# Kernel optimization log

Measured on AMD Instinct MI355X. Metric: run time of the kernel, lower is better.

Reference implementation:

```python
import jax, jax.numpy as jnp
import numpy as np

N_NODES = 100000
N_EDGES = 3200000
N_GRAPHS = 64
IN_DIM = 128
HID = 64
NUM_FAMILIES = 64
CPF = 3  # centroids per family
GOODWARE_C = 5
BN_EPS = 1e-5


def setup_inputs() -> dict:
    key = jax.random.key(0)
    ks = jax.random.split(key, 16)
    x = jax.random.normal(ks[0], (N_NODES, IN_DIM), dtype=jnp.float32)
    edge_index = jax.random.randint(ks[1], (2, N_EDGES), 0, N_NODES, dtype=jnp.int32)
    batch = jnp.sort(jax.random.randint(ks[2], (N_NODES,), 0, N_GRAPHS, dtype=jnp.int32))
    def lin(k, fin, fout):
        s = 1.0 / np.sqrt(fin)
        return jax.random.uniform(k, (fin, fout), jnp.float32, -s, s)
    W1 = lin(ks[3], IN_DIM, HID); b1 = jnp.zeros((HID,), jnp.float32)
    W2 = lin(ks[4], HID, HID);    b2 = jnp.zeros((HID,), jnp.float32)
    W3 = lin(ks[5], HID, HID);    b3 = jnp.zeros((HID,), jnp.float32)
    g1 = jnp.ones((HID,), jnp.float32); be1 = jnp.zeros((HID,), jnp.float32)
    g2 = jnp.ones((HID,), jnp.float32); be2 = jnp.zeros((HID,), jnp.float32)
    g3 = jnp.ones((HID,), jnp.float32); be3 = jnp.zeros((HID,), jnp.float32)
    cm = jax.random.normal(ks[6], (NUM_FAMILIES * CPF, HID), jnp.float32) / np.sqrt(HID)
    cg = jax.random.normal(ks[7], (GOODWARE_C, HID), jnp.float32) / np.sqrt(HID)
    temp = jnp.ones((1,), jnp.float32)
    return dict(x=x, edge_index=edge_index, batch=batch,
                W1=W1, b1=b1, g1=g1, be1=be1,
                W2=W2, b2=b2, g2=g2, be2=be2,
                W3=W3, b3=b3, g3=g3, be3=be3,
                cg=cg, cm=cm, temp=temp)


def _gcn_conv(h_in, W, b, row, col, dinv_sqrt):
    # GCNConv: lin -> symmetric-normalized scatter-add (with self loops) -> bias
    h = h_in @ W  # [N, HID]
    enorm = (dinv_sqrt[row] * dinv_sqrt[col])[:, None]  # [E, 1]
    agg = jax.ops.segment_sum(h[row] * enorm, col, num_segments=N_NODES)
    agg = agg + h * (dinv_sqrt * dinv_sqrt)[:, None]  # self-loop term (norm = 1/deg)
    return agg + b


def _bn(x, gamma, beta):
    # training-mode BatchNorm1d over node dim (biased variance)
    m = jnp.mean(x, axis=0)
    v = jnp.mean((x - m) ** 2, axis=0)
    return (x - m) * jax.lax.rsqrt(v + BN_EPS) * gamma + beta


def reference(x, edge_index, batch,
              W1, b1, g1, be1, W2, b2, g2, be2, W3, b3, g3, be3,
              cg, cm, temp):
    row, col = edge_index[0], edge_index[1]
    # degree including self loop
    deg = jax.ops.segment_sum(jnp.ones((N_EDGES,), jnp.float32), col,
                              num_segments=N_NODES) + 1.0
    dinv_sqrt = jax.lax.rsqrt(deg)

    h = jax.nn.relu(_bn(_gcn_conv(x, W1, b1, row, col, dinv_sqrt), g1, be1))
    h = jax.nn.relu(_bn(_gcn_conv(h, W2, b2, row, col, dinv_sqrt), g2, be2))
    h = _bn(_gcn_conv(h, W3, b3, row, col, dinv_sqrt), g3, be3)

    # global mean pool over graphs
    sums = jax.ops.segment_sum(h, batch, num_segments=N_GRAPHS)
    cnts = jax.ops.segment_sum(jnp.ones((N_NODES,), jnp.float32), batch,
                               num_segments=N_GRAPHS)
    emb = sums / jnp.maximum(cnts, 1.0)[:, None]  # [B, HID]

    # centroid classifier (phase='family')
    gd = jnp.sum((emb[:, None, :] - cg[None, :, :]) ** 2, axis=2)  # [B, 5]
    md = jnp.sum((emb[:, None, :] - cm[None, :, :]) ** 2, axis=2)  # [B, F*CPF]
    md = md.reshape(N_GRAPHS, NUM_FAMILIES, CPF)
    min_g = jnp.min(gd, axis=1)          # [B]
    min_m = jnp.min(md, axis=2)          # [B, F]
    logits = jnp.concatenate([(-min_g / temp)[:, None], -min_m / temp], axis=1)
    return logits
```

## Files before the change

### kernel.cpp

```cpp
#include <hip/hip_runtime.h>
#include <math.h>

#define N_NODES 100000
#define N_EDGES 3200000
#define N_GRAPHS 64
#define IN_DIM 128
#define HID 64
#define BN_EPS 1e-5f

#define PSHIFT 9
#define PBS 512
#define NPB ((N_NODES + PBS - 1) / PBS)
#define PART_BLOCKS 256
#define CHUNK_E (N_EDGES / PART_BLOCKS)

#define QBOUND 25000
#define AGG_BLOCKS 2048

typedef unsigned short ushort_t;
typedef __attribute__((ext_vector_type(8))) short bf16x8;
typedef __attribute__((ext_vector_type(4))) float f32x4;

__device__ __forceinline__ float bflo(unsigned u) { return __uint_as_float(u << 16); }
__device__ __forceinline__ float bfhi(unsigned u) { return __uint_as_float(u & 0xFFFF0000u); }
__device__ __forceinline__ float bfu(ushort_t u) { return __uint_as_float((unsigned)u << 16); }
__device__ __forceinline__ unsigned f2bf(float f) {
  unsigned u = __float_as_uint(f);
  return (u + 0x7FFFu + ((u >> 16) & 1u)) >> 16;
}


__global__ __launch_bounds__(256) void ghist_k(const int* __restrict__ ei,
                                               int* __restrict__ gh) {
  __shared__ int h[NPB];
  for (int i = threadIdx.x; i < NPB; i += 256) h[i] = 0;
  __syncthreads();
  const int4* d4 = (const int4*)(ei + N_EDGES);
  int n4 = N_EDGES / 4;
  int stride = gridDim.x * 256;
  for (int i = blockIdx.x * 256 + threadIdx.x; i < n4; i += stride) {
    int4 d = d4[i];
    atomicAdd(&h[d.x >> PSHIFT], 1);
    atomicAdd(&h[d.y >> PSHIFT], 1);
    atomicAdd(&h[d.z >> PSHIFT], 1);
    atomicAdd(&h[d.w >> PSHIFT], 1);
  }
  __syncthreads();
  for (int i = threadIdx.x; i < NPB; i += 256) {
    int v = h[i];
    if (v) atomicAdd(&gh[i], v);
  }
}

__global__ __launch_bounds__(256) void gscan_k(const int* __restrict__ gh,
                                               int* __restrict__ boff,
                                               int* __restrict__ gcur) {
  __shared__ int sa[256], sb[256];
  int t = threadIdx.x;
  int v = (t < NPB) ? gh[t] : 0;
  sa[t] = v;
  __syncthreads();
  int* src = sa; int* dst = sb;
  for (int o = 1; o < 256; o <<= 1) {
    dst[t] = src[t] + ((t >= o) ? src[t - o] : 0);
    __syncthreads();
    int* tmp = src; src = dst; dst = tmp;
  }
  if (t < NPB) {
    int excl = src[t] - v;
    boff[t] = excl;
    gcur[t] = excl;
    if (t == NPB - 1) boff[NPB] = src[t];
  }
}

__global__ __launch_bounds__(512) void part_k(const int* __restrict__ ei,
                                              int* __restrict__ gcur,
                                              unsigned* __restrict__ tmp) {
  __shared__ int lh[NPB];
  __shared__ int lcur[NPB];
  int t = threadIdx.x;
  for (int i = t; i < NPB; i += 512) lh[i] = 0;
  __syncthreads();
  int q0 = blockIdx.x * (CHUNK_E / 4);
  int q1 = q0 + CHUNK_E / 4;
  const int4* d4 = (const int4*)(ei + N_EDGES);
  const int4* s4 = (const int4*)ei;
  for (int i = q0 + t; i < q1; i += 512) {
    int4 d = d4[i];
    atomicAdd(&lh[d.x >> PSHIFT], 1);
    atomicAdd(&lh[d.y >> PSHIFT], 1);
    atomicAdd(&lh[d.z >> PSHIFT], 1);
    atomicAdd(&lh[d.w >> PSHIFT], 1);
  }
  __syncthreads();
  for (int i = t; i < NPB; i += 512) {
    int v = lh[i];
    lcur[i] = v ? atomicAdd(&gcur[i], v) : 0;
  }
  __syncthreads();
  for (int i = q0 + t; i < q1; i += 512) {
    int4 d = d4[i];
    int4 s = s4[i];
    int b0 = d.x >> PSHIFT, b1 = d.y >> PSHIFT, b2 = d.z >> PSHIFT, b3 = d.w >> PSHIFT;
    int p0 = atomicAdd(&lcur[b0], 1);
    int p1 = atomicAdd(&lcur[b1], 1);
    int p2 = atomicAdd(&lcur[b2], 1);
    int p3 = atomicAdd(&lcur[b3], 1);
    tmp[p0] = ((unsigned)(d.x & (PBS - 1)) << 17) | (unsigned)s.x;
    tmp[p1] = ((unsigned)(d.y & (PBS - 1)) << 17) | (unsigned)s.y;
    tmp[p2] = ((unsigned)(d.z & (PBS - 1)) << 17) | (unsigned)s.z;
    tmp[p3] = ((unsigned)(d.w & (PBS - 1)) << 17) | (unsigned)s.w;
  }
}

__global__ __launch_bounds__(512) void bwork_k(
    const unsigned* __restrict__ tmp, const int* __restrict__ boff,
    int* __restrict__ rp4, float* __restrict__ dinv, int* __restrict__ csr) {
  int b = blockIdx.x;
  int base = boff[b], end = boff[b + 1];
  int t = threadIdx.x;
  __shared__ int cnt[PBS * 4];
  __shared__ int cur[PBS * 4];
  __shared__ int sa[PBS], sb[PBS];
  for (int i = t; i < PBS * 4; i += 512) cnt[i] = 0;
  __syncthreads();
  int a0 = (base + 3) & ~3;
  int a1 = end & ~3;
  if (a1 < a0) { a0 = end; a1 = end; }
  const uint4* t4 = (const uint4*)tmp;
#define HIST1(U) { unsigned u_ = (U); int nl_ = u_ >> 17; int s_ = u_ & 0x1FFFF; \
    int qq_ = (s_ >= QBOUND) + (s_ >= 2*QBOUND) + (s_ >= 3*QBOUND); \
    atomicAdd(&cnt[nl_ * 4 + qq_], 1); }
  if (base + t < a0) HIST1(tmp[base + t]);
  for (int i = a0 / 4 + t; i < a1 / 4; i += 512) {
    uint4 u = t4[i];
    HIST1(u.x) HIST1(u.y) HIST1(u.z) HIST1(u.w)
  }
  if (a1 + t < end) HIST1(tmp[a1 + t]);
#undef HIST1
  __syncthreads();
  int c0 = cnt[t * 4], c1 = cnt[t * 4 + 1], c2 = cnt[t * 4 + 2], c3 = cnt[t * 4 + 3];
  int tsum = c0 + c1 + c2 + c3;
  sa[t] = tsum;
  __syncthreads();
  int* src_ = sa; int* dst_ = sb;
  for (int o = 1; o < PBS; o <<= 1) {
    dst_[t] = src_[t] + ((t >= o) ? src_[t - o] : 0);
    __syncthreads();
    int* z = src_; src_ = dst_; dst_ = z;
  }
  int nb = src_[t] - tsum;
  int o0 = nb, o1 = nb + c0, o2 = nb + c0 + c1, o3 = nb + c0 + c1 + c2;
  cur[t * 4] = o0; cur[t * 4 + 1] = o1; cur[t * 4 + 2] = o2; cur[t * 4 + 3] = o3;
  int n = b * PBS + t;
  if (n < N_NODES) {
    rp4[4 * n] = base + o0;
    rp4[4 * n + 1] = base + o1;
    rp4[4 * n + 2] = base + o2;
    rp4[4 * n + 3] = base + o3;
    dinv[n] = rsqrtf((float)(tsum + 1));
    if (n == N_NODES - 1) rp4[4 * N_NODES] = base + nb + tsum;
  }
  __syncthreads();
#define PLACE1(U) { unsigned u_ = (U); int nl_ = u_ >> 17; int s_ = u_ & 0x1FFFF; \
    int qq_ = (s_ >= QBOUND) + (s_ >= 2*QBOUND) + (s_ >= 3*QBOUND); \
    int p_ = atomicAdd(&cur[nl_ * 4 + qq_], 1); \
    csr[base + p_] = s_ << 7; }
  if (base + t < a0) PLACE1(tmp[base + t]);
  for (int i = a0 / 4 + t; i < a1 / 4; i += 512) {
    uint4 u = t4[i];
    PLACE1(u.x) PLACE1(u.y) PLACE1(u.z) PLACE1(u.w)
  }
  if (a1 + t < end) PLACE1(tmp[a1 + t]);
#undef PLACE1
}


template <int K, bool XBF16, bool APPLY, bool RELU>
__global__ __launch_bounds__(256) void gemm_k(
    const void* __restrict__ Xv, const float* __restrict__ W,
    const float* __restrict__ sums, const float* __restrict__ gamma,
    const float* __restrict__ beta, const float* __restrict__ dinv,
    ushort_t* __restrict__ out, int nrows) {
  __shared__ ushort_t wt[64 * K];
  __shared__ float scs[128], shs[128];
  __shared__ float redo[64 * 65];
  const int tid = threadIdx.x;
  const int wv = tid >> 6;
  const int lane = tid & 63;
  const int lm = lane & 15;
  const int lq = lane >> 4;

  for (int idx = tid; idx < K * 64; idx += 256) {
    int k = idx >> 6, c = idx & 63;
    wt[c * K + k] = (ushort_t)f2bf(W[idx]);
  }
  if (APPLY) {
    for (int k = tid; k < K; k += 256) {
      float m = sums[k] / (float)N_NODES;
      float v = sums[64 + k] / (float)N_NODES - m * m;
      float s = gamma[k] * rsqrtf(v + BN_EPS);
      scs[k] = s;
      shs[k] = beta[k] - m * s;
    }
  }
  __syncthreads();

  const int rowbase = blockIdx.x * 64;
  const int grow = rowbase + wv * 16 + lm;
  const bool valid = grow < nrows;
  f32x4 acc0 = {0.f, 0.f, 0.f, 0.f};
  f32x4 acc1 = acc0, acc2 = acc0, acc3 = acc0;

#pragma unroll
  for (int k0 = 0; k0 < K; k0 += 32) {
    int kbase = k0 + lq * 8;
    bf16x8 a = {0, 0, 0, 0, 0, 0, 0, 0};
    if (valid) {
      if (XBF16) {
        uint4 u = *(const uint4*)((const char*)Xv + ((size_t)grow * 64 + kbase) * 2);
        if (APPLY) {
          float4 sc0 = *(const float4*)&scs[kbase];
          float4 sc1 = *(const float4*)&scs[kbase + 4];
          float4 sh0 = *(const float4*)&shs[kbase];
          float4 sh1 = *(const float4*)&shs[kbase + 4];
          float f0 = bflo(u.x) * sc0.x + sh0.x, f1 = bfhi(u.x) * sc0.y + sh0.y;
          float f2 = bflo(u.y) * sc0.z + sh0.z, f3 = bfhi(u.y) * sc0.w + sh0.w;
          float f4 = bflo(u.z) * sc1.x + sh1.x, f5 = bfhi(u.z) * sc1.y + sh1.y;
          float f6 = bflo(u.w) * sc1.z + sh1.z, f7 = bfhi(u.w) * sc1.w + sh1.w;
          if (RELU) {
            f0 = fmaxf(f0, 0.f); f1 = fmaxf(f1, 0.f);
            f2 = fmaxf(f2, 0.f); f3 = fmaxf(f3, 0.f);
            f4 = fmaxf(f4, 0.f); f5 = fmaxf(f5, 0.f);
            f6 = fmaxf(f6, 0.f); f7 = fmaxf(f7, 0.f);
          }
          a[0] = (short)f2bf(f0); a[1] = (short)f2bf(f1);
          a[2] = (short)f2bf(f2); a[3] = (short)f2bf(f3);
          a[4] = (short)f2bf(f4); a[5] = (short)f2bf(f5);
          a[6] = (short)f2bf(f6); a[7] = (short)f2bf(f7);
        } else {
          a = *(const bf16x8*)&u;
        }
      } else {
        const float* xp = (const float*)Xv + (size_t)grow * K + kbase;
        float4 xa = *(const float4*)xp;
        float4 xb = *(const float4*)(xp + 4);
        a[0] = (short)f2bf(xa.x); a[1] = (short)f2bf(xa.y);
        a[2] = (short)f2bf(xa.z); a[3] = (short)f2bf(xa.w);
        a[4] = (short)f2bf(xb.x); a[5] = (short)f2bf(xb.y);
        a[6] = (short)f2bf(xb.z); a[7] = (short)f2bf(xb.w);
      }
    }
    bf16x8 b0 = *(const bf16x8*)(wt + (0 + lm) * K + kbase);
    bf16x8 b1 = *(const bf16x8*)(wt + (16 + lm) * K + kbase);
    bf16x8 b2 = *(const bf16x8*)(wt + (32 + lm) * K + kbase);
    bf16x8 b3 = *(const bf16x8*)(wt + (48 + lm) * K + kbase);
    acc0 = __builtin_amdgcn_mfma_f32_16x16x32_bf16(a, b0, acc0, 0, 0, 0);
    acc1 = __builtin_amdgcn_mfma_f32_16x16x32_bf16(a, b1, acc1, 0, 0, 0);
    acc2 = __builtin_amdgcn_mfma_f32_16x16x32_bf16(a, b2, acc2, 0, 0, 0);
    acc3 = __builtin_amdgcn_mfma_f32_16x16x32_bf16(a, b3, acc3, 0, 0, 0);
  }

#pragma unroll
  for (int r = 0; r < 4; ++r) {
    int rr = wv * 16 + lq * 4 + r;
    redo[rr * 65 + lm] = acc0[r];
    redo[rr * 65 + 16 + lm] = acc1[r];
    redo[rr * 65 + 32 + lm] = acc2[r];
    redo[rr * 65 + 48 + lm] = acc3[r];
  }
  __syncthreads();
  {
    int r = tid >> 2;
    int cq = (tid & 3) * 16;
    int gr = rowbase + r;
    if (gr < nrows) {
      float dn = dinv[gr];
      const float* sp = &redo[r * 65 + cq];
      unsigned p[8];
#pragma unroll
      for (int i = 0; i < 8; ++i)
        p[i] = f2bf(sp[2 * i] * dn) | (f2bf(sp[2 * i + 1] * dn) << 16);
      char* ob = (char*)out + ((size_t)gr * 64 + cq) * 2;
      *(uint4*)ob = make_uint4(p[0], p[1], p[2], p[3]);
      *(uint4*)(ob + 16) = make_uint4(p[4], p[5], p[6], p[7]);
    }
  }
}


__global__ __launch_bounds__(256) void agg_k(
    const ushort_t* __restrict__ hs, const float* __restrict__ dinv,
    const int* __restrict__ rp4, const int* __restrict__ csr,
    const float* __restrict__ bias, ushort_t* __restrict__ out,
    float* __restrict__ sums) {
  const int tid = threadIdx.x;
  const int w = tid >> 6;
  const int lane = tid & 63;
  const int g = lane >> 4;
  const int q = lane & 15;
  const char* hb = (const char*)hs;
  char* ob = (char*)out;

  float4 bval = *(const float4*)(bias + q * 4);
  float4 s = make_float4(0.f, 0.f, 0.f, 0.f);
  float4 s2 = make_float4(0.f, 0.f, 0.f, 0.f);

  for (int n = blockIdx.x * 16 + w * 4 + g; n < N_NODES; n += AGG_BLOCKS * 16) {
    int r0 = rp4[4 * n];
    int cnt = rp4[4 * n + 4] - r0;
    uint2 selfu = *(const uint2*)(hb + ((size_t)n << 7) + (q << 3));
    float4 aA = {0, 0, 0, 0}, aB = {0, 0, 0, 0};
    int j = 0;
    if (cnt >= 8) {
      int e0 = csr[r0 + 0], e1 = csr[r0 + 1], e2 = csr[r0 + 2], e3 = csr[r0 + 3];
      int e4 = csr[r0 + 4], e5 = csr[r0 + 5], e6 = csr[r0 + 6], e7 = csr[r0 + 7];
      for (; j + 16 <= cnt; j += 8) {
        uint2 v0 = *(const uint2*)(hb + (size_t)(unsigned)e0 + (q << 3));
        uint2 v1 = *(const uint2*)(hb + (size_t)(unsigned)e1 + (q << 3));
        uint2 v2 = *(const uint2*)(hb + (size_t)(unsigned)e2 + (q << 3));
        uint2 v3 = *(const uint2*)(hb + (size_t)(unsigned)e3 + (q << 3));
        uint2 v4 = *(const uint2*)(hb + (size_t)(unsigned)e4 + (q << 3));
        uint2 v5 = *(const uint2*)(hb + (size_t)(unsigned)e5 + (q << 3));
        uint2 v6 = *(const uint2*)(hb + (size_t)(unsigned)e6 + (q << 3));
        uint2 v7 = *(const uint2*)(hb + (size_t)(unsigned)e7 + (q << 3));
        e0 = csr[r0 + j + 8];  e1 = csr[r0 + j + 9];
        e2 = csr[r0 + j + 10]; e3 = csr[r0 + j + 11];
        e4 = csr[r0 + j + 12]; e5 = csr[r0 + j + 13];
        e6 = csr[r0 + j + 14]; e7 = csr[r0 + j + 15];
        aA.x += bflo(v0.x); aA.y += bfhi(v0.x); aA.z += bflo(v0.y); aA.w += bfhi(v0.y);
        aB.x += bflo(v1.x); aB.y += bfhi(v1.x); aB.z += bflo(v1.y); aB.w += bfhi(v1.y);
        aA.x += bflo(v2.x); aA.y += bfhi(v2.x); aA.z += bflo(v2.y); aA.w += bfhi(v2.y);
        aB.x += bflo(v3.x); aB.y += bfhi(v3.x); aB.z += bflo(v3.y); aB.w += bfhi(v3.y);
        aA.x += bflo(v4.x); aA.y += bfhi(v4.x); aA.z += bflo(v4.y); aA.w += bfhi(v4.y);
        aB.x += bflo(v5.x); aB.y += bfhi(v5.x); aB.z += bflo(v5.y); aB.w += bfhi(v5.y);
        aA.x += bflo(v6.x); aA.y += bfhi(v6.x); aA.z += bflo(v6.y); aA.w += bfhi(v6.y);
        aB.x += bflo(v7.x); aB.y += bfhi(v7.x); aB.z += bflo(v7.y); aB.w += bfhi(v7.y);
      }
      {
        uint2 v0 = *(const uint2*)(hb + (size_t)(unsigned)e0 + (q << 3));
        uint2 v1 = *(const uint2*)(hb + (size_t)(unsigned)e1 + (q << 3));
        uint2 v2 = *(const uint2*)(hb + (size_t)(unsigned)e2 + (q << 3));
        uint2 v3 = *(const uint2*)(hb + (size_t)(unsigned)e3 + (q << 3));
        uint2 v4 = *(const uint2*)(hb + (size_t)(unsigned)e4 + (q << 3));
        uint2 v5 = *(const uint2*)(hb + (size_t)(unsigned)e5 + (q << 3));
        uint2 v6 = *(const uint2*)(hb + (size_t)(unsigned)e6 + (q << 3));
        uint2 v7 = *(const uint2*)(hb + (size_t)(unsigned)e7 + (q << 3));
        aA.x += bflo(v0.x); aA.y += bfhi(v0.x); aA.z += bflo(v0.y); aA.w += bfhi(v0.y);
        aB.x += bflo(v1.x); aB.y += bfhi(v1.x); aB.z += bflo(v1.y); aB.w += bfhi(v1.y);
        aA.x += bflo(v2.x); aA.y += bfhi(v2.x); aA.z += bflo(v2.y); aA.w += bfhi(v2.y);
        aB.x += bflo(v3.x); aB.y += bfhi(v3.x); aB.z += bflo(v3.y); aB.w += bfhi(v3.y);
        aA.x += bflo(v4.x); aA.y += bfhi(v4.x); aA.z += bflo(v4.y); aA.w += bfhi(v4.y);
        aB.x += bflo(v5.x); aB.y += bfhi(v5.x); aB.z += bflo(v5.y); aB.w += bfhi(v5.y);
        aA.x += bflo(v6.x); aA.y += bfhi(v6.x); aA.z += bflo(v6.y); aA.w += bfhi(v6.y);
        aB.x += bflo(v7.x); aB.y += bfhi(v7.x); aB.z += bflo(v7.y); aB.w += bfhi(v7.y);
        j += 8;
      }
    }
    for (; j + 2 <= cnt; j += 2) {
      int e0 = csr[r0 + j + 0], e1 = csr[r0 + j + 1];
      uint2 v0 = *(const uint2*)(hb + (size_t)(unsigned)e0 + (q << 3));
      uint2 v1 = *(const uint2*)(hb + (size_t)(unsigned)e1 + (q << 3));
      aA.x += bflo(v0.x); aA.y += bfhi(v0.x); aA.z += bflo(v0.y); aA.w += bfhi(v0.y);
      aB.x += bflo(v1.x); aB.y += bfhi(v1.x); aB.z += bflo(v1.y); aB.w += bfhi(v1.y);
    }
    if (j < cnt) {
      int e0 = csr[r0 + j];
      uint2 v0 = *(const uint2*)(hb + (size_t)(unsigned)e0 + (q << 3));
      aA.x += bflo(v0.x); aA.y += bfhi(v0.x); aA.z += bflo(v0.y); aA.w += bfhi(v0.y);
    }
    float4 a;
    a.x = aA.x + aB.x + bflo(selfu.x);
    a.y = aA.y + aB.y + bfhi(selfu.x);
    a.z = aA.z + aB.z + bflo(selfu.y);
    a.w = aA.w + aB.w + bfhi(selfu.y);
    float dn = dinv[n];
    a.x = a.x * dn + bval.x; a.y = a.y * dn + bval.y;
    a.z = a.z * dn + bval.z; a.w = a.w * dn + bval.w;
    uint2 o;
    o.x = f2bf(a.x) | (f2bf(a.y) << 16);
    o.y = f2bf(a.z) | (f2bf(a.w) << 16);
    *(uint2*)(ob + ((size_t)n << 7) + (q << 3)) = o;
    s.x += a.x; s.y += a.y; s.z += a.z; s.w += a.w;
    s2.x += a.x * a.x; s2.y += a.y * a.y;
    s2.z += a.z * a.z; s2.w += a.w * a.w;
  }

  __shared__ float rs[16][64];
  __shared__ float rs2[16][64];
  *(float4*)(&rs[w * 4 + g][q * 4]) = s;
  *(float4*)(&rs2[w * 4 + g][q * 4]) = s2;
  __syncthreads();
  int c = tid & 63;
  int r0_ = tid >> 6;
  float a = rs[r0_][c] + rs[r0_ + 4][c] + rs[r0_ + 8][c] + rs[r0_ + 12][c];
  float a2 = rs2[r0_][c] + rs2[r0_ + 4][c] + rs2[r0_ + 8][c] + rs2[r0_ + 12][c];
  __syncthreads();
  rs[r0_][c] = a;
  rs2[r0_][c] = a2;
  __syncthreads();
  if (r0_ == 0) {
    atomicAdd(&sums[c], rs[0][c] + rs[1][c] + rs[2][c] + rs[3][c]);
    atomicAdd(&sums[64 + c], rs2[0][c] + rs2[1][c] + rs2[2][c] + rs2[3][c]);
  }
}


#define POOL_CHUNK 32
__global__ __launch_bounds__(256) void pool_k(
    const ushort_t* __restrict__ h, const float* __restrict__ sums,
    const float* __restrict__ gamma, const float* __restrict__ beta,
    const int* __restrict__ batch,
    float* __restrict__ psum, float* __restrict__ pcnt) {
  int w = threadIdx.x >> 6;
  int lane = threadIdx.x & 63;
  int start = (blockIdx.x * 4 + w) * POOL_CHUNK;
  if (start >= N_NODES) return;
  int end = min(start + POOL_CHUNK, N_NODES);
  float m = sums[lane] / (float)N_NODES;
  float v = sums[64 + lane] / (float)N_NODES - m * m;
  float sc = gamma[lane] * rsqrtf(v + BN_EPS);
  float sh = beta[lane] - m * sc;
  float acc = 0.f, cnt = 0.f;
  int cur = batch[start];
  for (int n = start; n < end; ++n) {
    int g = batch[n];
    if (g != cur) {
      atomicAdd(&psum[cur * 64 + lane], acc);
      if (lane == 0) atomicAdd(&pcnt[cur], cnt);
      acc = 0.f; cnt = 0.f; cur = g;
    }
    acc += bfu(h[(size_t)n * 64 + lane]) * sc + sh;
    cnt += 1.f;
  }
  atomicAdd(&psum[cur * 64 + lane], acc);
  if (lane == 0) atomicAdd(&pcnt[cur], cnt);
}


__global__ void classify_k(const float* __restrict__ psum, const float* __restrict__ pcnt,
                           const float* __restrict__ cg_, const float* __restrict__ cm,
                           const float* __restrict__ temp, float* __restrict__ out) {
  int g = blockIdx.x;
  int t = threadIdx.x;
  __shared__ float emb[64];
  __shared__ float dist[208];
  if (t < 64) emb[t] = psum[g * 64 + t] / fmaxf(pcnt[g], 1.0f);
  __syncthreads();
  if (t < 197) {
    const float* C = (t < 5) ? (cg_ + t * 64) : (cm + (t - 5) * 64);
    float d = 0.f;
#pragma unroll 8
    for (int k = 0; k < 64; ++k) {
      float df = emb[k] - C[k];
      d += df * df;
    }
    dist[t] = d;
  }
  __syncthreads();
  float tv = temp[0];
  if (t == 64) {
    float m = dist[0];
    for (int j = 1; j < 5; ++j) m = fminf(m, dist[j]);
    out[g * 65] = -m / tv;
  }
  if (t < 64) {
    float m = fminf(dist[5 + t * 3], fminf(dist[5 + t * 3 + 1], dist[5 + t * 3 + 2]));
    out[g * 65 + 1 + t] = -m / tv;
  }
}


extern "C" void kernel_launch(void* const* d_in, const int* in_sizes, int n_in,
                              void* d_out, int out_size, void* d_ws, size_t ws_size,
                              hipStream_t stream) {
  const float* x   = (const float*)d_in[0];
  const int* ei    = (const int*)d_in[1];
  const int* batch = (const int*)d_in[2];
  const float* W1 = (const float*)d_in[3];  const float* b1 = (const float*)d_in[4];
  const float* g1 = (const float*)d_in[5];  const float* be1 = (const float*)d_in[6];
  const float* W2 = (const float*)d_in[7];  const float* b2 = (const float*)d_in[8];
  const float* g2 = (const float*)d_in[9];  const float* be2 = (const float*)d_in[10];
  const float* W3 = (const float*)d_in[11]; const float* b3 = (const float*)d_in[12];
  const float* g3 = (const float*)d_in[13]; const float* be3 = (const float*)d_in[14];
  const float* cg_ = (const float*)d_in[15];
  const float* cm = (const float*)d_in[16];
  const float* temp = (const float*)d_in[17];
  float* out = (float*)d_out;

  char* ws = (char*)d_ws;
  size_t off = 0;
  auto alloc = [&](size_t bytes) -> void* {
    void* p = ws + off;
    off = (off + bytes + 255) & ~(size_t)255;
    return p;
  };
  int* gh        = (int*)alloc((size_t)NPB * 4);
  float* sumsAll = (float*)alloc(3 * 128 * 4);
  float* psum    = (float*)alloc(64 * 64 * 4);
  float* pcnt    = (float*)alloc(64 * 4);
  size_t zero_end = off;
  int* boff      = (int*)alloc((size_t)(NPB + 1) * 4);
  int* gcur      = (int*)alloc((size_t)NPB * 4);
  unsigned* tmp  = (unsigned*)alloc((size_t)N_EDGES * 4);
  int* csr       = (int*)alloc((size_t)N_EDGES * 4);
  int* rp4       = (int*)alloc((size_t)(4 * N_NODES + 1) * 4);
  float* dinv    = (float*)alloc((size_t)N_NODES * 4);
  ushort_t* hA   = (ushort_t*)alloc((size_t)N_NODES * 64 * 2);
  ushort_t* hB   = (ushort_t*)alloc((size_t)N_NODES * 64 * 2);

  hipMemsetAsync(ws, 0, zero_end, stream);

  const int NB_GEMM = (N_NODES + 63) / 64;
  const int NB_POOL = (N_NODES + POOL_CHUNK * 4 - 1) / (POOL_CHUNK * 4);

  ghist_k<<<512, 256, 0, stream>>>(ei, gh);
  gscan_k<<<1, 256, 0, stream>>>(gh, boff, gcur);
  part_k<<<PART_BLOCKS, 512, 0, stream>>>(ei, gcur, tmp);
  bwork_k<<<NPB, 512, 0, stream>>>(tmp, boff, rp4, dinv, csr);

  gemm_k<IN_DIM, false, false, false><<<NB_GEMM, 256, 0, stream>>>(x, W1, nullptr, nullptr, nullptr, dinv, hA, N_NODES);
  agg_k<<<AGG_BLOCKS, 256, 0, stream>>>(hA, dinv, rp4, csr, b1, hB, sumsAll);

  gemm_k<HID, true, true, true><<<NB_GEMM, 256, 0, stream>>>(hB, W2, sumsAll, g1, be1, dinv, hA, N_NODES);
  agg_k<<<AGG_BLOCKS, 256, 0, stream>>>(hA, dinv, rp4, csr, b2, hB, sumsAll + 128);

  gemm_k<HID, true, true, true><<<NB_GEMM, 256, 0, stream>>>(hB, W3, sumsAll + 128, g2, be2, dinv, hA, N_NODES);
  agg_k<<<AGG_BLOCKS, 256, 0, stream>>>(hA, dinv, rp4, csr, b3, hB, sumsAll + 256);

  pool_k<<<NB_POOL, 256, 0, stream>>>(hB, sumsAll + 256, g3, be3, batch, psum, pcnt);
  classify_k<<<N_GRAPHS, 256, 0, stream>>>(psum, pcnt, cg_, cm, temp, out);
}
```

Baseline: 545.0 us.

## Fuse pooling into last aggregation and restructure agg to per-thread node batches

The aggregation kernel now assigns four consecutive nodes to each 16-lane group, using one block per 64 nodes instead of a grid-stride loop. It reads the four partitioned row-pointer ranges with vector loads and walks each partition with an 8/4/2/1 unrolled gather. The final layer's aggregation accumulates per-graph sums into shared memory and flushes them with atomics, so the separate pool kernel and the write of the last hidden state go away. The BatchNorm affine is applied to the pooled mean in the classifier, since it is linear. The trade-offs are a 16KB shared buffer with its zeroing in the pooled variant, and loss of the two-accumulator software prefetching in the gather loop.

```diff
diff --git a/kernel.cpp b/kernel.cpp
--- a/kernel.cpp
+++ b/kernel.cpp
@@ -15,7 +15,7 @@
 #define CHUNK_E (N_EDGES / PART_BLOCKS)
 
 #define QBOUND 25000
-#define AGG_BLOCKS 2048
+#define NB_AGG ((N_NODES + 63) / 64)
 
 typedef unsigned short ushort_t;
 typedef __attribute__((ext_vector_type(8))) short bf16x8;
@@ -290,11 +290,13 @@
 }
 
 
+template <bool POOL>
 __global__ __launch_bounds__(256) void agg_k(
     const ushort_t* __restrict__ hs, const float* __restrict__ dinv,
     const int* __restrict__ rp4, const int* __restrict__ csr,
     const float* __restrict__ bias, ushort_t* __restrict__ out,
-    float* __restrict__ sums) {
+    float* __restrict__ sums, const int* __restrict__ batch,
+    float* __restrict__ psum, float* __restrict__ pcnt) {
   const int tid = threadIdx.x;
   const int w = tid >> 6;
   const int lane = tid & 63;
@@ -302,93 +304,147 @@
   const int q = lane & 15;
   const char* hb = (const char*)hs;
   char* ob = (char*)out;
-
+  const int qo = q << 3;
+
+  __shared__ float rs[16][64];
+  __shared__ float rs2[16][64];
+  __shared__ float pl[POOL ? 64 * 64 : 1];
+  __shared__ float pcl[POOL ? 64 : 1];
+  if (POOL) {
+    for (int i = tid; i < 64 * 64; i += 256) pl[i] = 0.f;
+    if (tid < 64) pcl[tid] = 0.f;
+    __syncthreads();
+  }
+
+  const int nb = blockIdx.x * 64 + (w * 4 + g) * 4;
+
+  int4 rp[4];
+  int en[4];
+#pragma unroll
+  for (int i = 0; i < 4; ++i) {
+    int n = nb + i;
+    if (n < N_NODES) {
+      rp[i] = *(const int4*)(rp4 + 4 * n);
+      en[i] = rp4[4 * n + 4];
+    } else {
+      rp[i] = make_int4(0, 0, 0, 0);
+      en[i] = 0;
+    }
+  }
   float4 bval = *(const float4*)(bias + q * 4);
+  float4 acc[4];
+#pragma unroll
+  for (int i = 0; i < 4; ++i) acc[i] = make_float4(0.f, 0.f, 0.f, 0.f);
+
+#define GV1(E, A) { uint2 v_ = *(const uint2*)(hb + (size_t)(unsigned)(E) + qo); \
+    A.x += bflo(v_.x); A.y += bfhi(v_.x); A.z += bflo(v_.y); A.w += bfhi(v_.y); }
+
+  for (int p = 0; p < 4; ++p) {
+#pragma unroll
+    for (int i = 0; i < 4; ++i) {
+      int lo = (p == 0) ? rp[i].x : (p == 1) ? rp[i].y : (p == 2) ? rp[i].z : rp[i].w;
+      int hi = (p == 3) ? en[i] : ((p == 0) ? rp[i].y : (p == 1) ? rp[i].z : rp[i].w);
+      float4 a4 = acc[i];
+      int jj = lo;
+      for (; jj + 8 <= hi; jj += 8) {
+        int e0 = csr[jj], e1 = csr[jj + 1], e2 = csr[jj + 2], e3 = csr[jj + 3];
+        int e4 = csr[jj + 4], e5 = csr[jj + 5], e6 = csr[jj + 6], e7 = csr[jj + 7];
+        uint2 v0 = *(const uint2*)(hb + (size_t)(unsigned)e0 + qo);
+        uint2 v1 = *(const uint2*)(hb + (size_t)(unsigned)e1 + qo);
+        uint2 v2 = *(const uint2*)(hb + (size_t)(unsigned)e2 + qo);
+        uint2 v3 = *(const uint2*)(hb + (size_t)(unsigned)e3 + qo);
+        uint2 v4 = *(const uint2*)(hb + (size_t)(unsigned)e4 + qo);
+        uint2 v5 = *(const uint2*)(hb + (size_t)(unsigned)e5 + qo);
+        uint2 v6 = *(const uint2*)(hb + (size_t)(unsigned)e6 + qo);
+        uint2 v7 = *(const uint2*)(hb + (size_t)(unsigned)e7 + qo);
+        a4.x += bflo(v0.x); a4.y += bfhi(v0.x); a4.z += bflo(v0.y); a4.w += bfhi(v0.y);
+        a4.x += bflo(v1.x); a4.y += bfhi(v1.x); a4.z += bflo(v1.y); a4.w += bfhi(v1.y);
+        a4.x += bflo(v2.x); a4.y += bfhi(v2.x); a4.z += bflo(v2.y); a4.w += bfhi(v2.y);
+        a4.x += bflo(v3.x); a4.y += bfhi(v3.x); a4.z += bflo(v3.y); a4.w += bfhi(v3.y);
+        a4.x += bflo(v4.x); a4.y += bfhi(v4.x); a4.z += bflo(v4.y); a4.w += bfhi(v4.y);
+        a4.x += bflo(v5.x); a4.y += bfhi(v5.x); a4.z += bflo(v5.y); a4.w += bfhi(v5.y);
+        a4.x += bflo(v6.x); a4.y += bfhi(v6.x); a4.z += bflo(v6.y); a4.w += bfhi(v6.y);
+        a4.x += bflo(v7.x); a4.y += bfhi(v7.x); a4.z += bflo(v7.y); a4.w += bfhi(v7.y);
+      }
+      if (jj + 4 <= hi) {
+        int e0 = csr[jj], e1 = csr[jj + 1], e2 = csr[jj + 2], e3 = csr[jj + 3];
+        uint2 v0 = *(const uint2*)(hb + (size_t)(unsigned)e0 + qo);
+        uint2 v1 = *(const uint2*)(hb + (size_t)(unsigned)e1 + qo);
+        uint2 v2 = *(const uint2*)(hb + (size_t)(unsigned)e2 + qo);
+        uint2 v3 = *(const uint2*)(hb + (size_t)(unsigned)e3 + qo);
+        a4.x += bflo(v0.x); a4.y += bfhi(v0.x); a4.z += bflo(v0.y); a4.w += bfhi(v0.y);
+        a4.x += bflo(v1.x); a4.y += bfhi(v1.x); a4.z += bflo(v1.y); a4.w += bfhi(v1.y);
+        a4.x += bflo(v2.x); a4.y += bfhi(v2.x); a4.z += bflo(v2.y); a4.w += bfhi(v2.y);
+        a4.x += bflo(v3.x); a4.y += bfhi(v3.x); a4.z += bflo(v3.y); a4.w += bfhi(v3.y);
+        jj += 4;
+      }
+      if (jj + 2 <= hi) {
+        int e0 = csr[jj], e1 = csr[jj + 1];
+        uint2 v0 = *(const uint2*)(hb + (size_t)(unsigned)e0 + qo);
+        uint2 v1 = *(const uint2*)(hb + (size_t)(unsigned)e1 + qo);
+        a4.x += bflo(v0.x); a4.y += bfhi(v0.x); a4.z += bflo(v0.y); a4.w += bfhi(v0.y);
+        a4.x += bflo(v1.x); a4.y += bfhi(v1.x); a4.z += bflo(v1.y); a4.w += bfhi(v1.y);
+        jj += 2;
+      }
+      if (jj < hi) {
+        GV1(csr[jj], a4)
+      }
+      acc[i] = a4;
+    }
+  }
+#undef GV1
+
   float4 s = make_float4(0.f, 0.f, 0.f, 0.f);
   float4 s2 = make_float4(0.f, 0.f, 0.f, 0.f);
-
-  for (int n = blockIdx.x * 16 + w * 4 + g; n < N_NODES; n += AGG_BLOCKS * 16) {
-    int r0 = rp4[4 * n];
-    int cnt = rp4[4 * n + 4] - r0;
-    uint2 selfu = *(const uint2*)(hb + ((size_t)n << 7) + (q << 3));
-    float4 aA = {0, 0, 0, 0}, aB = {0, 0, 0, 0};
-    int j = 0;
-    if (cnt >= 8) {
-      int e0 = csr[r0 + 0], e1 = csr[r0 + 1], e2 = csr[r0 + 2], e3 = csr[r0 + 3];
-      int e4 = csr[r0 + 4], e5 = csr[r0 + 5], e6 = csr[r0 + 6], e7 = csr[r0 + 7];
-      for (; j + 16 <= cnt; j += 8) {
-        uint2 v0 = *(const uint2*)(hb + (size_t)(unsigned)e0 + (q << 3));
-        uint2 v1 = *(const uint2*)(hb + (size_t)(unsigned)e1 + (q << 3));
-        uint2 v2 = *(const uint2*)(hb + (size_t)(unsigned)e2 + (q << 3));
-        uint2 v3 = *(const uint2*)(hb + (size_t)(unsigned)e3 + (q << 3));
-        uint2 v4 = *(const uint2*)(hb + (size_t)(unsigned)e4 + (q << 3));
-        uint2 v5 = *(const uint2*)(hb + (size_t)(unsigned)e5 + (q << 3));
-        uint2 v6 = *(const uint2*)(hb + (size_t)(unsigned)e6 + (q << 3));
-        uint2 v7 = *(const uint2*)(hb + (size_t)(unsigned)e7 + (q << 3));
-        e0 = csr[r0 + j + 8];  e1 = csr[r0 + j + 9];
-        e2 = csr[r0 + j + 10]; e3 = csr[r0 + j + 11];
-        e4 = csr[r0 + j + 12]; e5 = csr[r0 + j + 13];
-        e6 = csr[r0 + j + 14]; e7 = csr[r0 + j + 15];
-        aA.x += bflo(v0.x); aA.y += bfhi(v0.x); aA.z += bflo(v0.y); aA.w += bfhi(v0.y);
-        aB.x += bflo(v1.x); aB.y += bfhi(v1.x); aB.z += bflo(v1.y); aB.w += bfhi(v1.y);
-        aA.x += bflo(v2.x); aA.y += bfhi(v2.x); aA.z += bflo(v2.y); aA.w += bfhi(v2.y);
-        aB.x += bflo(v3.x); aB.y += bfhi(v3.x); aB.z += bflo(v3.y); aB.w += bfhi(v3.y);
-        aA.x += bflo(v4.x); aA.y += bfhi(v4.x); aA.z += bflo(v4.y); aA.w += bfhi(v4.y);
-        aB.x += bflo(v5.x); aB.y += bfhi(v5.x); aB.z += bflo(v5.y); aB.w += bfhi(v5.y);
-        aA.x += bflo(v6.x); aA.y += bfhi(v6.x); aA.z += bflo(v6.y); aA.w += bfhi(v6.y);
-        aB.x += bflo(v7.x); aB.y += bfhi(v7.x); aB.z += bflo(v7.y); aB.w += bfhi(v7.y);
+  int curg = -1, pcount = 0;
+  float4 pacc = make_float4(0.f, 0.f, 0.f, 0.f);
+#pragma unroll
+  for (int i = 0; i < 4; ++i) {
+    int n = nb + i;
+    if (n < N_NODES) {
+      uint2 su = *(const uint2*)(hb + ((size_t)n << 7) + qo);
+      float dn = dinv[n];
+      float4 a;
+      a.x = (acc[i].x + bflo(su.x)) * dn + bval.x;
+      a.y = (acc[i].y + bfhi(su.x)) * dn + bval.y;
+      a.z = (acc[i].z + bflo(su.y)) * dn + bval.z;
+      a.w = (acc[i].w + bfhi(su.y)) * dn + bval.w;
+      if (!POOL) {
+        uint2 o;
+        o.x = f2bf(a.x) | (f2bf(a.y) << 16);
+        o.y = f2bf(a.z) | (f2bf(a.w) << 16);
+        *(uint2*)(ob + ((size_t)n << 7) + qo) = o;
+      } else {
+        int gi = batch[n];
+        if (gi != curg) {
+          if (pcount) {
+            atomicAdd(&pl[curg * 64 + (q << 2)], pacc.x);
+            atomicAdd(&pl[curg * 64 + (q << 2) + 1], pacc.y);
+            atomicAdd(&pl[curg * 64 + (q << 2) + 2], pacc.z);
+            atomicAdd(&pl[curg * 64 + (q << 2) + 3], pacc.w);
+            if (q == 0) atomicAdd(&pcl[curg], (float)pcount);
+          }
+          curg = gi;
+          pacc = a;
+          pcount = 1;
+        } else {
+          pacc.x += a.x; pacc.y += a.y; pacc.z += a.z; pacc.w += a.w;
+          pcount++;
+        }
       }
-      {
-        uint2 v0 = *(const uint2*)(hb + (size_t)(unsigned)e0 + (q << 3));
-        uint2 v1 = *(const uint2*)(hb + (size_t)(unsigned)e1 + (q << 3));
-        uint2 v2 = *(const uint2*)(hb + (size_t)(unsigned)e2 + (q << 3));
-        uint2 v3 = *(const uint2*)(hb + (size_t)(unsigned)e3 + (q << 3));
-        uint2 v4 = *(const uint2*)(hb + (size_t)(unsigned)e4 + (q << 3));
-        uint2 v5 = *(const uint2*)(hb + (size_t)(unsigned)e5 + (q << 3));
-        uint2 v6 = *(const uint2*)(hb + (size_t)(unsigned)e6 + (q << 3));
-        uint2 v7 = *(const uint2*)(hb + (size_t)(unsigned)e7 + (q << 3));
-        aA.x += bflo(v0.x); aA.y += bfhi(v0.x); aA.z += bflo(v0.y); aA.w += bfhi(v0.y);
-        aB.x += bflo(v1.x); aB.y += bfhi(v1.x); aB.z += bflo(v1.y); aB.w += bfhi(v1.y);
-        aA.x += bflo(v2.x); aA.y += bfhi(v2.x); aA.z += bflo(v2.y); aA.w += bfhi(v2.y);
-        aB.x += bflo(v3.x); aB.y += bfhi(v3.x); aB.z += bflo(v3.y); aB.w += bfhi(v3.y);
-        aA.x += bflo(v4.x); aA.y += bfhi(v4.x); aA.z += bflo(v4.y); aA.w += bfhi(v4.y);
-        aB.x += bflo(v5.x); aB.y += bfhi(v5.x); aB.z += bflo(v5.y); aB.w += bfhi(v5.y);
-        aA.x += bflo(v6.x); aA.y += bfhi(v6.x); aA.z += bflo(v6.y); aA.w += bfhi(v6.y);
-        aB.x += bflo(v7.x); aB.y += bfhi(v7.x); aB.z += bflo(v7.y); aB.w += bfhi(v7.y);
-        j += 8;
-      }
-    }
-    for (; j + 2 <= cnt; j += 2) {
-      int e0 = csr[r0 + j + 0], e1 = csr[r0 + j + 1];
-      uint2 v0 = *(const uint2*)(hb + (size_t)(unsigned)e0 + (q << 3));
-      uint2 v1 = *(const uint2*)(hb + (size_t)(unsigned)e1 + (q << 3));
-      aA.x += bflo(v0.x); aA.y += bfhi(v0.x); aA.z += bflo(v0.y); aA.w += bfhi(v0.y);
-      aB.x += bflo(v1.x); aB.y += bfhi(v1.x); aB.z += bflo(v1.y); aB.w += bfhi(v1.y);
-    }
-    if (j < cnt) {
-      int e0 = csr[r0 + j];
-      uint2 v0 = *(const uint2*)(hb + (size_t)(unsigned)e0 + (q << 3));
-      aA.x += bflo(v0.x); aA.y += bfhi(v0.x); aA.z += bflo(v0.y); aA.w += bfhi(v0.y);
-    }
-    float4 a;
-    a.x = aA.x + aB.x + bflo(selfu.x);
-    a.y = aA.y + aB.y + bfhi(selfu.x);
-    a.z = aA.z + aB.z + bflo(selfu.y);
-    a.w = aA.w + aB.w + bfhi(selfu.y);
-    float dn = dinv[n];
-    a.x = a.x * dn + bval.x; a.y = a.y * dn + bval.y;
-    a.z = a.z * dn + bval.z; a.w = a.w * dn + bval.w;
-    uint2 o;
-    o.x = f2bf(a.x) | (f2bf(a.y) << 16);
-    o.y = f2bf(a.z) | (f2bf(a.w) << 16);
-    *(uint2*)(ob + ((size_t)n << 7) + (q << 3)) = o;
-    s.x += a.x; s.y += a.y; s.z += a.z; s.w += a.w;
-    s2.x += a.x * a.x; s2.y += a.y * a.y;
-    s2.z += a.z * a.z; s2.w += a.w * a.w;
-  }
-
-  __shared__ float rs[16][64];
-  __shared__ float rs2[16][64];
+      s.x += a.x; s.y += a.y; s.z += a.z; s.w += a.w;
+      s2.x += a.x * a.x; s2.y += a.y * a.y;
+      s2.z += a.z * a.z; s2.w += a.w * a.w;
+    }
+  }
+  if (POOL && pcount) {
+    atomicAdd(&pl[curg * 64 + (q << 2)], pacc.x);
+    atomicAdd(&pl[curg * 64 + (q << 2) + 1], pacc.y);
+    atomicAdd(&pl[curg * 64 + (q << 2) + 2], pacc.z);
+    atomicAdd(&pl[curg * 64 + (q << 2) + 3], pacc.w);
+    if (q == 0) atomicAdd(&pcl[curg], (float)pcount);
+  }
+
   *(float4*)(&rs[w * 4 + g][q * 4]) = s;
   *(float4*)(&rs2[w * 4 + g][q * 4]) = s2;
   __syncthreads();
@@ -404,49 +460,32 @@
     atomicAdd(&sums[c], rs[0][c] + rs[1][c] + rs[2][c] + rs[3][c]);
     atomicAdd(&sums[64 + c], rs2[0][c] + rs2[1][c] + rs2[2][c] + rs2[3][c]);
   }
-}
-
-
-#define POOL_CHUNK 32
-__global__ __launch_bounds__(256) void pool_k(
-    const ushort_t* __restrict__ h, const float* __restrict__ sums,
-    const float* __restrict__ gamma, const float* __restrict__ beta,
-    const int* __restrict__ batch,
-    float* __restrict__ psum, float* __restrict__ pcnt) {
-  int w = threadIdx.x >> 6;
-  int lane = threadIdx.x & 63;
-  int start = (blockIdx.x * 4 + w) * POOL_CHUNK;
-  if (start >= N_NODES) return;
-  int end = min(start + POOL_CHUNK, N_NODES);
-  float m = sums[lane] / (float)N_NODES;
-  float v = sums[64 + lane] / (float)N_NODES - m * m;
-  float sc = gamma[lane] * rsqrtf(v + BN_EPS);
-  float sh = beta[lane] - m * sc;
-  float acc = 0.f, cnt = 0.f;
-  int cur = batch[start];
-  for (int n = start; n < end; ++n) {
-    int g = batch[n];
-    if (g != cur) {
-      atomicAdd(&psum[cur * 64 + lane], acc);
-      if (lane == 0) atomicAdd(&pcnt[cur], cnt);
-      acc = 0.f; cnt = 0.f; cur = g;
-    }
-    acc += bfu(h[(size_t)n * 64 + lane]) * sc + sh;
-    cnt += 1.f;
-  }
-  atomicAdd(&psum[cur * 64 + lane], acc);
-  if (lane == 0) atomicAdd(&pcnt[cur], cnt);
+  if (POOL) {
+    for (int idx = tid; idx < 64 * 64; idx += 256) {
+      int gi = idx >> 6;
+      if (pcl[gi] != 0.f) atomicAdd(&psum[idx], pl[idx]);
+    }
+    if (tid < 64 && pcl[tid] != 0.f) atomicAdd(&pcnt[tid], pcl[tid]);
+  }
 }
 
 
 __global__ void classify_k(const float* __restrict__ psum, const float* __restrict__ pcnt,
+                           const float* __restrict__ sums, const float* __restrict__ gamma,
+                           const float* __restrict__ beta,
                            const float* __restrict__ cg_, const float* __restrict__ cm,
                            const float* __restrict__ temp, float* __restrict__ out) {
   int g = blockIdx.x;
   int t = threadIdx.x;
   __shared__ float emb[64];
   __shared__ float dist[208];
-  if (t < 64) emb[t] = psum[g * 64 + t] / fmaxf(pcnt[g], 1.0f);
+  if (t < 64) {
+    float m = sums[t] / (float)N_NODES;
+    float v = sums[64 + t] / (float)N_NODES - m * m;
+    float sc = gamma[t] * rsqrtf(v + BN_EPS);
+    float sh = beta[t] - m * sc;
+    emb[t] = psum[g * 64 + t] / fmaxf(pcnt[g], 1.0f) * sc + sh;
+  }
   __syncthreads();
   if (t < 197) {
     const float* C = (t < 5) ? (cg_ + t * 64) : (cm + (t - 5) * 64);
@@ -513,7 +552,6 @@
   hipMemsetAsync(ws, 0, zero_end, stream);
 
   const int NB_GEMM = (N_NODES + 63) / 64;
-  const int NB_POOL = (N_NODES + POOL_CHUNK * 4 - 1) / (POOL_CHUNK * 4);
 
   ghist_k<<<512, 256, 0, stream>>>(ei, gh);
   gscan_k<<<1, 256, 0, stream>>>(gh, boff, gcur);
@@ -521,14 +559,13 @@
   bwork_k<<<NPB, 512, 0, stream>>>(tmp, boff, rp4, dinv, csr);
 
   gemm_k<IN_DIM, false, false, false><<<NB_GEMM, 256, 0, stream>>>(x, W1, nullptr, nullptr, nullptr, dinv, hA, N_NODES);
-  agg_k<<<AGG_BLOCKS, 256, 0, stream>>>(hA, dinv, rp4, csr, b1, hB, sumsAll);
+  agg_k<false><<<NB_AGG, 256, 0, stream>>>(hA, dinv, rp4, csr, b1, hB, sumsAll, nullptr, nullptr, nullptr);
 
   gemm_k<HID, true, true, true><<<NB_GEMM, 256, 0, stream>>>(hB, W2, sumsAll, g1, be1, dinv, hA, N_NODES);
-  agg_k<<<AGG_BLOCKS, 256, 0, stream>>>(hA, dinv, rp4, csr, b2, hB, sumsAll + 128);
+  agg_k<false><<<NB_AGG, 256, 0, stream>>>(hA, dinv, rp4, csr, b2, hB, sumsAll + 128, nullptr, nullptr, nullptr);
 
   gemm_k<HID, true, true, true><<<NB_GEMM, 256, 0, stream>>>(hB, W3, sumsAll + 128, g2, be2, dinv, hA, N_NODES);
-  agg_k<<<AGG_BLOCKS, 256, 0, stream>>>(hA, dinv, rp4, csr, b3, hB, sumsAll + 256);
-
-  pool_k<<<NB_POOL, 256, 0, stream>>>(hB, sumsAll + 256, g3, be3, batch, psum, pcnt);
-  classify_k<<<N_GRAPHS, 256, 0, stream>>>(psum, pcnt, cg_, cm, temp, out);
-}
+  agg_k<true><<<NB_AGG, 256, 0, stream>>>(hA, dinv, rp4, csr, b3, nullptr, sumsAll + 256, batch, psum, pcnt);
+
+  classify_k<<<N_GRAPHS, 256, 0, stream>>>(psum, pcnt, sumsAll + 256, g3, be3, cg_, cm, temp, out);
+}
```

New measurement: 647.0 us. 18.7% more time.
